# Kernel tuning notes

Measured on AMD Instinct MI355X. Metric: run time of the kernel, lower is better.

The kernel has to match this reference:

```python
import jax, jax.numpy as jnp
import numpy as np

LATDIM = 128
ANCHOR_SET_NUM = 64
N_NODES = 10000

def setup_inputs() -> dict:
    key = jax.random.key(0)
    k1, k2, k3, k4, k5 = jax.random.split(key, 5)
    embeds = jax.random.normal(k1, (N_NODES, LATDIM), dtype=jnp.float32)
    dists_array = jax.random.uniform(k2, (ANCHOR_SET_NUM, N_NODES), dtype=jnp.float32)
    W_hidden = jax.random.normal(k3, (LATDIM, 2 * LATDIM), dtype=jnp.float32) * 0.05
    b_hidden = jax.random.normal(k4, (LATDIM,), dtype=jnp.float32) * 0.05
    anchorset_id = jax.random.randint(k5, (ANCHOR_SET_NUM,), 0, N_NODES, dtype=jnp.int64 if jax.config.jax_enable_x64 else jnp.int32)
    return {"embeds": embeds, "dists_array": dists_array, "W_hidden": W_hidden,
            "b_hidden": b_hidden, "anchorset_id": anchorset_id}

def reference(embeds, dists_array, W_hidden, b_hidden, anchorset_id):
    A, N = dists_array.shape
    d = embeds.shape[1]
    set_ids_emb = embeds[anchorset_id]                       # [A, d] anchor gather
    # messages[i, j] = set_ids_emb[j] * dists[j, i]
    messages = set_ids_emb[None, :, :] * dists_array.T[:, :, None]   # [N, A, d]
    # faithful to torch: embeds.repeat(A,1).reshape(-1, A, d) -> embeds[(i*A+j) % N]
    self_feature = jnp.tile(embeds, (A, 1)).reshape(N, A, d)          # [N, A, d]
    m = jnp.concatenate([messages, self_feature], axis=-1)            # [N, A, 2d]
    h = jnp.einsum('nak,ok->nao', m, W_hidden) + b_hidden             # [N, A, d]
    return jnp.mean(h, axis=1)                                        # [N, d]
```

## Files before the change

kernel.cpp:

```cpp
#include <hip/hip_runtime.h>

#define LATDIM 128
#define ANUM   64
#define NNODES 10000
#define PERIOD 625
#define TN     32
#define PPB    8
#define PBLK   (ANUM / PPB)
#define TBLK   157
#define WP4    33


__global__ __launch_bounds__(256) void prep_kernel(
    const float* __restrict__ embeds,
    const float* __restrict__ W,
    const float* __restrict__ b,
    const int*   __restrict__ anchor,
    float* __restrict__ P,
    float* __restrict__ T2b)
{
    __shared__ float W_s[128 * 4 * WP4];
    __shared__ float X_s[PPB * LATDIM];
    __shared__ float R_s[PPB * LATDIM];
    const int tid = threadIdx.x;
    const bool isP = (blockIdx.x < PBLK);
    const int off = isP ? 0 : LATDIM;
    float4* W_s4 = (float4*)W_s;
    const float4* X_s4 = (const float4*)X_s;
    const int col = tid & 127;
    const int h   = tid >> 7;

    #pragma unroll
    for (int it = 0; it < 16; ++it) {
        int f = it * 256 + tid;
        int r = f >> 5, c4 = f & 31;
        W_s4[r * WP4 + c4] =
            *(const float4*)(W + r * (2 * LATDIM) + off + 4 * c4);
    }

    if (isP) {
        const int a0 = blockIdx.x * PPB;
        #pragma unroll
        for (int it = 0; it < 4; ++it) {
            int idx = it * 256 + tid;
            int j = idx >> 7, c = idx & 127;
            X_s[j * LATDIM + c] = embeds[(size_t)anchor[a0 + j] * LATDIM + c];
        }
        __syncthreads();

        float acc[PPB] = {};
        #pragma unroll
        for (int k4 = 0; k4 < 16; ++k4) {
            int kk = h * 16 + k4;
            float4 w = W_s4[col * WP4 + kk];
            #pragma unroll
            for (int j = 0; j < PPB; ++j) {
                float4 e = X_s4[j * 32 + kk];
                acc[j] += e.x*w.x + e.y*w.y + e.z*w.z + e.w*w.w;
            }
        }
        if (h == 1) {
            #pragma unroll
            for (int j = 0; j < PPB; ++j) R_s[j * LATDIM + col] = acc[j];
        }
        __syncthreads();
        if (h == 0) {
            #pragma unroll
            for (int j = 0; j < PPB; ++j)
                P[(size_t)(a0 + j) * LATDIM + col] =
                    acc[j] + R_s[j * LATDIM + col];
        }
    } else {
        const int t = blockIdx.x - PBLK;
        const int rbase = 64 * t;
        float acc[4] = {};
        #define LDROW(r_) ({ int row_ = rbase + (r_);                        \
                             if (row_ >= NNODES) row_ -= NNODES;             \
                             embeds[(size_t)row_ * LATDIM + col]; })
        #pragma unroll
        for (int i = 0; i < 24; ++i) {
            acc[0] += LDROW(h + 2 * i);
        }
        #pragma unroll
        for (int i = 0; i < 8; ++i) {
            float v = LDROW(48 + h + 2 * i); acc[0] += v; acc[1] += v;
        }
        #pragma unroll
        for (int i = 0; i < 16; ++i) {
            acc[1] += LDROW(64 + h + 2 * i);
        }
        #pragma unroll
        for (int i = 0; i < 8; ++i) {
            float v = LDROW(96 + h + 2 * i); acc[1] += v; acc[2] += v;
        }
        #pragma unroll
        for (int i = 0; i < 16; ++i) {
            acc[2] += LDROW(112 + h + 2 * i);
        }
        #pragma unroll
        for (int i = 0; i < 8; ++i) {
            float v = LDROW(144 + h + 2 * i); acc[2] += v; acc[3] += v;
        }
        #pragma unroll
        for (int i = 0; i < 24; ++i) {
            acc[3] += LDROW(160 + h + 2 * i);
        }
        #undef LDROW

        if (h == 1) {
            #pragma unroll
            for (int j = 0; j < 4; ++j) R_s[j * LATDIM + col] = acc[j];
        }
        __syncthreads();
        if (h == 0) {
            #pragma unroll
            for (int j = 0; j < 4; ++j)
                X_s[j * LATDIM + col] = acc[j] + R_s[j * LATDIM + col];
        }
        __syncthreads();

        float acc2[4] = {};
        #pragma unroll
        for (int k4 = 0; k4 < 16; ++k4) {
            int kk = h * 16 + k4;
            float4 w = W_s4[col * WP4 + kk];
            #pragma unroll
            for (int j = 0; j < 4; ++j) {
                float4 s = X_s4[j * 32 + kk];
                acc2[j] += s.x*w.x + s.y*w.y + s.z*w.z + s.w*w.w;
            }
        }
        if (h == 1) {
            #pragma unroll
            for (int j = 0; j < 4; ++j) R_s[j * LATDIM + col] = acc2[j];
        }
        __syncthreads();
        if (h == 0) {
            const float bias = b[col];
            #pragma unroll
            for (int j = 0; j < 4; ++j) {
                int s = t + 157 * j;
                if (s < PERIOD)
                    T2b[(size_t)s * LATDIM + col] =
                        bias + (acc2[j] + R_s[j * LATDIM + col]) * (1.0f / ANUM);
            }
        }
    }
}

__global__ __launch_bounds__(256) void main_kernel(
    const float* __restrict__ dists,
    const float* __restrict__ P,
    const float* __restrict__ T2b,
    float* __restrict__ out)
{
    __shared__ float P_s[ANUM * LATDIM];
    const int tid = threadIdx.x;

    {
        float4* P_s4 = (float4*)P_s;
        const float4* Pg = (const float4*)P;
        #pragma unroll
        for (int it = 0; it < (ANUM * LATDIM / 4) / 256; ++it)
            P_s4[it * 256 + tid] = Pg[it * 256 + tid];
    }
    __syncthreads();

    const int lane = tid & 63;
    const int w    = __builtin_amdgcn_readfirstlane(tid >> 6);
    const int o    = (w & 1) * 64 + lane;
    const int nc   = w >> 1;
    int nb = blockIdx.x * TN + nc * 16;
    const bool live = (nb + 16) <= NNODES;
    if (!live) nb = NNODES - 16;

    float acc[16] = {};
    for (int a = 0; a < ANUM; ++a) {
        const float p = P_s[a * LATDIM + o];
        const float* __restrict__ drow = dists + (size_t)a * NNODES + nb;
        #pragma unroll
        for (int j = 0; j < 16; ++j)
            acc[j] += drow[j] * p;
    }

    if (live) {
        #pragma unroll
        for (int j = 0; j < 16; ++j) {
            const int n = nb + j;
            const int s = n % PERIOD;
            out[(size_t)n * LATDIM + o] =
                acc[j] * (1.0f / ANUM) + T2b[(size_t)s * LATDIM + o];
        }
    }
}

extern "C" void kernel_launch(void* const* d_in, const int* in_sizes, int n_in,
                              void* d_out, int out_size, void* d_ws, size_t ws_size,
                              hipStream_t stream) {
    const float* embeds = (const float*)d_in[0];
    const float* dists  = (const float*)d_in[1];
    const float* W      = (const float*)d_in[2];
    const float* b      = (const float*)d_in[3];
    const int*   anchor = (const int*)d_in[4];
    float* out = (float*)d_out;

    float* P   = (float*)d_ws;
    float* T2b = P + ANUM * LATDIM;

    prep_kernel<<<PBLK + TBLK, 256, 0, stream>>>(embeds, W, b, anchor, P, T2b);
    main_kernel<<<(NNODES + TN - 1) / TN, 256, 0, stream>>>(dists, P, T2b, out);
}
```

Measured before the change: 80.32 us.

## Split prep into per-anchor and per-residue blocks and halve main-kernel node tile

The prep kernel now launches one block per anchor and one block per residue class (689 blocks instead of 165). Each block reads W directly from global memory rather than staging a padded W tile in shared memory, and the self-feature window sums use float4 loads. The main kernel processes 8 nodes per wave instead of 16, giving 625 blocks and no tail handling, with the anchor loop partially unrolled. The aim is more parallelism and less per-block shared-memory setup. The cost is redundant global reads of W across many more blocks, and each main-kernel block now reloads all of P into shared memory for half as many nodes.

```diff
diff --git a/kernel.cpp b/kernel.cpp
--- a/kernel.cpp
+++ b/kernel.cpp
@@ -4,11 +4,9 @@
 #define ANUM   64
 #define NNODES 10000
 #define PERIOD 625
-#define TN     32
-#define PPB    8
-#define PBLK   (ANUM / PPB)
-#define TBLK   157
-#define WP4    33
+#define TN     16
+#define ABLK   64
+#define SBLK   625
 
 
 __global__ __launch_bounds__(256) void prep_kernel(
@@ -19,132 +17,73 @@
     float* __restrict__ P,
     float* __restrict__ T2b)
 {
-    __shared__ float W_s[128 * 4 * WP4];
-    __shared__ float X_s[PPB * LATDIM];
-    __shared__ float R_s[PPB * LATDIM];
+    __shared__ float X_s[LATDIM];
+    __shared__ float R_s[LATDIM];
+    __shared__ float Xp[8][LATDIM];
     const int tid = threadIdx.x;
-    const bool isP = (blockIdx.x < PBLK);
-    const int off = isP ? 0 : LATDIM;
-    float4* W_s4 = (float4*)W_s;
     const float4* X_s4 = (const float4*)X_s;
-    const int col = tid & 127;
-    const int h   = tid >> 7;
 
-    #pragma unroll
-    for (int it = 0; it < 16; ++it) {
-        int f = it * 256 + tid;
-        int r = f >> 5, c4 = f & 31;
-        W_s4[r * WP4 + c4] =
-            *(const float4*)(W + r * (2 * LATDIM) + off + 4 * c4);
-    }
-
-    if (isP) {
-        const int a0 = blockIdx.x * PPB;
-        #pragma unroll
-        for (int it = 0; it < 4; ++it) {
-            int idx = it * 256 + tid;
-            int j = idx >> 7, c = idx & 127;
-            X_s[j * LATDIM + c] = embeds[(size_t)anchor[a0 + j] * LATDIM + c];
+    if (blockIdx.x < ABLK) {
+        const int a = blockIdx.x;
+        if (tid < 32) {
+            ((float4*)X_s)[tid] =
+                *((const float4*)(embeds + (size_t)anchor[a] * LATDIM) + tid);
         }
         __syncthreads();
 
-        float acc[PPB] = {};
+        const int o = tid & 127;
+        const int h = tid >> 7;
+        const float4* Wr = (const float4*)(W + (size_t)o * (2 * LATDIM) + h * 64);
+        float acc = 0.f;
         #pragma unroll
         for (int k4 = 0; k4 < 16; ++k4) {
-            int kk = h * 16 + k4;
-            float4 w = W_s4[col * WP4 + kk];
-            #pragma unroll
-            for (int j = 0; j < PPB; ++j) {
-                float4 e = X_s4[j * 32 + kk];
-                acc[j] += e.x*w.x + e.y*w.y + e.z*w.z + e.w*w.w;
-            }
+            float4 w4 = Wr[k4];
+            float4 x4 = X_s4[h * 16 + k4];
+            acc += w4.x * x4.x + w4.y * x4.y + w4.z * x4.z + w4.w * x4.w;
         }
-        if (h == 1) {
-            #pragma unroll
-            for (int j = 0; j < PPB; ++j) R_s[j * LATDIM + col] = acc[j];
-        }
+        if (h == 1) R_s[o] = acc;
         __syncthreads();
-        if (h == 0) {
-            #pragma unroll
-            for (int j = 0; j < PPB; ++j)
-                P[(size_t)(a0 + j) * LATDIM + col] =
-                    acc[j] + R_s[j * LATDIM + col];
-        }
+        if (h == 0) P[(size_t)a * LATDIM + o] = acc + R_s[o];
     } else {
-        const int t = blockIdx.x - PBLK;
-        const int rbase = 64 * t;
-        float acc[4] = {};
-        #define LDROW(r_) ({ int row_ = rbase + (r_);                        \
-                             if (row_ >= NNODES) row_ -= NNODES;             \
-                             embeds[(size_t)row_ * LATDIM + col]; })
-        #pragma unroll
-        for (int i = 0; i < 24; ++i) {
-            acc[0] += LDROW(h + 2 * i);
-        }
+        const int s = blockIdx.x - ABLK;
+        const int row0 = (64 * s) % NNODES;
+
+        const int c4 = tid & 31;
+        const int hg = tid >> 5;
+        float4 sum = {0.f, 0.f, 0.f, 0.f};
         #pragma unroll
         for (int i = 0; i < 8; ++i) {
-            float v = LDROW(48 + h + 2 * i); acc[0] += v; acc[1] += v;
+            int row = row0 + 8 * i + hg;
+            if (row >= NNODES) row -= NNODES;
+            float4 v = *((const float4*)(embeds + (size_t)row * LATDIM) + c4);
+            sum.x += v.x; sum.y += v.y; sum.z += v.z; sum.w += v.w;
         }
-        #pragma unroll
-        for (int i = 0; i < 16; ++i) {
-            acc[1] += LDROW(64 + h + 2 * i);
-        }
-        #pragma unroll
-        for (int i = 0; i < 8; ++i) {
-            float v = LDROW(96 + h + 2 * i); acc[1] += v; acc[2] += v;
-        }
-        #pragma unroll
-        for (int i = 0; i < 16; ++i) {
-            acc[2] += LDROW(112 + h + 2 * i);
-        }
-        #pragma unroll
-        for (int i = 0; i < 8; ++i) {
-            float v = LDROW(144 + h + 2 * i); acc[2] += v; acc[3] += v;
-        }
-        #pragma unroll
-        for (int i = 0; i < 24; ++i) {
-            acc[3] += LDROW(160 + h + 2 * i);
-        }
-        #undef LDROW
-
-        if (h == 1) {
+        ((float4*)&Xp[hg][0])[c4] = sum;
+        __syncthreads();
+        if (tid < LATDIM) {
+            float t = Xp[0][tid];
             #pragma unroll
-            for (int j = 0; j < 4; ++j) R_s[j * LATDIM + col] = acc[j];
-        }
-        __syncthreads();
-        if (h == 0) {
-            #pragma unroll
-            for (int j = 0; j < 4; ++j)
-                X_s[j * LATDIM + col] = acc[j] + R_s[j * LATDIM + col];
+            for (int g = 1; g < 8; ++g) t += Xp[g][tid];
+            X_s[tid] = t;
         }
         __syncthreads();
 
-        float acc2[4] = {};
+        const int o = tid & 127;
+        const int h = tid >> 7;
+        const float4* Wr =
+            (const float4*)(W + (size_t)o * (2 * LATDIM) + LATDIM + h * 64);
+        float acc = 0.f;
         #pragma unroll
         for (int k4 = 0; k4 < 16; ++k4) {
-            int kk = h * 16 + k4;
-            float4 w = W_s4[col * WP4 + kk];
-            #pragma unroll
-            for (int j = 0; j < 4; ++j) {
-                float4 s = X_s4[j * 32 + kk];
-                acc2[j] += s.x*w.x + s.y*w.y + s.z*w.z + s.w*w.w;
-            }
+            float4 w4 = Wr[k4];
+            float4 x4 = X_s4[h * 16 + k4];
+            acc += w4.x * x4.x + w4.y * x4.y + w4.z * x4.z + w4.w * x4.w;
         }
-        if (h == 1) {
-            #pragma unroll
-            for (int j = 0; j < 4; ++j) R_s[j * LATDIM + col] = acc2[j];
-        }
+        if (h == 1) R_s[o] = acc;
         __syncthreads();
-        if (h == 0) {
-            const float bias = b[col];
-            #pragma unroll
-            for (int j = 0; j < 4; ++j) {
-                int s = t + 157 * j;
-                if (s < PERIOD)
-                    T2b[(size_t)s * LATDIM + col] =
-                        bias + (acc2[j] + R_s[j * LATDIM + col]) * (1.0f / ANUM);
-            }
-        }
+        if (h == 0)
+            T2b[(size_t)s * LATDIM + o] =
+                b[o] + (acc + R_s[o]) * (1.0f / ANUM);
     }
 }
 
@@ -170,27 +109,24 @@
     const int w    = __builtin_amdgcn_readfirstlane(tid >> 6);
     const int o    = (w & 1) * 64 + lane;
     const int nc   = w >> 1;
-    int nb = blockIdx.x * TN + nc * 16;
-    const bool live = (nb + 16) <= NNODES;
-    if (!live) nb = NNODES - 16;
+    const int nb   = blockIdx.x * TN + nc * 8;
 
-    float acc[16] = {};
+    float acc[8] = {};
+    #pragma unroll 4
     for (int a = 0; a < ANUM; ++a) {
         const float p = P_s[a * LATDIM + o];
         const float* __restrict__ drow = dists + (size_t)a * NNODES + nb;
         #pragma unroll
-        for (int j = 0; j < 16; ++j)
+        for (int j = 0; j < 8; ++j)
             acc[j] += drow[j] * p;
     }
 
-    if (live) {
-        #pragma unroll
-        for (int j = 0; j < 16; ++j) {
-            const int n = nb + j;
-            const int s = n % PERIOD;
-            out[(size_t)n * LATDIM + o] =
-                acc[j] * (1.0f / ANUM) + T2b[(size_t)s * LATDIM + o];
-        }
+    #pragma unroll
+    for (int j = 0; j < 8; ++j) {
+        const int n = nb + j;
+        const int s = n % PERIOD;
+        out[(size_t)n * LATDIM + o] =
+            acc[j] * (1.0f / ANUM) + T2b[(size_t)s * LATDIM + o];
     }
 }
 
@@ -207,6 +143,6 @@
     float* P   = (float*)d_ws;
     float* T2b = P + ANUM * LATDIM;
 
-    prep_kernel<<<PBLK + TBLK, 256, 0, stream>>>(embeds, W, b, anchor, P, T2b);
-    main_kernel<<<(NNODES + TN - 1) / TN, 256, 0, stream>>>(dists, P, T2b, out);
+    prep_kernel<<<ABLK + SBLK, 256, 0, stream>>>(embeds, W, b, anchor, P, T2b);
+    main_kernel<<<NNODES / TN, 256, 0, stream>>>(dists, P, T2b, out);
 }
```

New measurement: 82.37 us. 1.03x slower.
